# Kernel optimization log

Measured on AMD Instinct MI355X. Metric: run time of the kernel, lower is better.

## Reference

```python
import jax, jax.numpy as jnp
import numpy as np
import math

B, S, D, H = 2, 2048, 1024, 16
DH = D // H  # dim_per_head = 64


def setup_inputs() -> dict:
    key = jax.random.key(0)
    ks = jax.random.split(key, 12)
    s = 1.0 / math.sqrt(D)
    return {
        "key": jax.random.normal(ks[0], (B, S, D), jnp.float32),
        "value": jax.random.normal(ks[1], (B, S, D), jnp.float32),
        "query": jax.random.normal(ks[2], (B, S, D), jnp.float32),
        "mask": jax.random.randint(ks[3], (B, S, S), 0, 2).astype(bool),
        "Wq": jax.random.normal(ks[4], (D, D), jnp.float32) * s,
        "bq": jnp.zeros((D,), jnp.float32),
        "Wk": jax.random.normal(ks[5], (D, D), jnp.float32) * s,
        "bk": jnp.zeros((D,), jnp.float32),
        "Wv": jax.random.normal(ks[6], (D, D), jnp.float32) * s,
        "bv": jnp.zeros((D,), jnp.float32),
        "Wo": jax.random.normal(ks[7], (D, D), jnp.float32) * s,
        "bo": jnp.zeros((D,), jnp.float32),
    }


def _shape(x):
    # [B, S, D] -> [B, H, S, DH]
    return x.reshape(B, -1, H, DH).transpose(0, 2, 1, 3)


def reference(key, value, query, mask, Wq, bq, Wk, bk, Wv, bv, Wo, bo):
    q = _shape(query @ Wq.T + bq)  # [B,H,Sq,DH]
    k = _shape(key @ Wk.T + bk)    # [B,H,Sk,DH]
    v = _shape(value @ Wv.T + bv)  # [B,H,Sk,DH]
    q = q / jnp.sqrt(jnp.asarray(DH, q.dtype))
    scores = jnp.einsum("bhqd,bhkd->bhqk", q, k)
    scores = jnp.where(mask[:, None, :, :], jnp.asarray(-1e18, scores.dtype), scores)
    attn = jax.nn.softmax(scores, axis=-1)
    # dropout is identity in eval/deterministic reference
    ctx = jnp.einsum("bhqk,bhkd->bhqd", attn, v)
    ctx = ctx.transpose(0, 2, 1, 3).reshape(B, -1, D)  # unshape
    return ctx @ Wo.T + bo
```

## Files before the change

### kernel.cpp

```cpp
#include <hip/hip_runtime.h>
#include <math.h>


constexpr int Bc  = 2;
constexpr int Sc  = 2048;
constexpr int Dc  = 1024;
constexpr int Hc  = 16;
constexpr int DHc = 64;
constexpr int BSc = Bc * Sc;

constexpr float LOG2E = 1.4426950408889634f;

typedef __bf16 bf16x8 __attribute__((ext_vector_type(8)));
typedef __bf16 bf16x4 __attribute__((ext_vector_type(4)));
typedef float  f32x4  __attribute__((ext_vector_type(4)));

#define GLDS16(gp, lp) __builtin_amdgcn_global_load_lds( \
    (const __attribute__((address_space(1))) void*)(gp), \
    (__attribute__((address_space(3))) void*)(lp), 16, 0, 0)

__global__ __launch_bounds__(256)
void wsplit(const float* __restrict__ W0, const float* __restrict__ W1,
            const float* __restrict__ W2, const float* __restrict__ W3,
            __bf16* __restrict__ out)
{
    const float* src[4] = {W0, W1, W2, W3};
    const int z = blockIdx.y;
    const size_t idx = ((size_t)blockIdx.x * 256 + threadIdx.x) * 4;
    const float4 v = *(const float4*)&src[z][idx];
    bf16x4 o;
    o[0] = (__bf16)v.x; o[1] = (__bf16)v.y; o[2] = (__bf16)v.z; o[3] = (__bf16)v.w;
    *(bf16x4*)&out[(size_t)z * Dc * Dc + idx] = o;
}

__device__ __forceinline__ void sweep128p(const float* __restrict__ A,
                                          const __bf16* __restrict__ Wh,
                                          char* AsB, char* WsB,
                                          int gm0, int gn0, f32x4 acc[4][4])
{
    const int tid  = threadIdx.x;
    const int w    = tid >> 6;
    const int lane = tid & 63;
    const int cc   = lane & 15;
    const int g    = lane >> 4;
    const int wm   = (w & 1) * 64;
    const int wn   = (w >> 1) * 64;

    int wrow[4], wchk[4];
#pragma unroll
    for (int r = 0; r < 4; ++r) {
        const int L = r * 256 + tid;
        wrow[r] = L >> 3;
        wchk[r] = (L & 7) ^ (wrow[r] & 7);
    }

    float4 av[8];
#pragma unroll
    for (int r = 0; r < 4; ++r)
        GLDS16(Wh + (size_t)(gn0 + wrow[r]) * Dc + wchk[r] * 8,
               WsB + (r * 256 + tid) * 16);
#pragma unroll
    for (int i = 0; i < 8; ++i) {
        const int Lq = i * 256 + tid;
        av[i] = *(const float4*)&A[(size_t)(gm0 + (Lq >> 4)) * Dc + (Lq & 15) * 4];
    }
#pragma unroll
    for (int i = 0; i < 8; ++i) {
        const int Lq = i * 256 + tid;
        const int ar = Lq >> 4, aq = Lq & 15;
        const int off = ar * 128 + ((((aq >> 1) ^ (ar & 7)) << 4) | ((aq & 1) << 3));
        bf16x4 hv;
        hv[0] = (__bf16)av[i].x; hv[1] = (__bf16)av[i].y;
        hv[2] = (__bf16)av[i].z; hv[3] = (__bf16)av[i].w;
        *(bf16x4*)(AsB + off) = hv;
    }

    for (int it = 0; it < Dc / 64; ++it) {
        const char* As = AsB + (it & 1) * 16384;
        const char* Ws = WsB + (it & 1) * 16384;
        __syncthreads();

        const bool more = (it + 1 < Dc / 64);
        if (more) {
            const int kn = (it + 1) * 64;
            char* Wn = WsB + ((it + 1) & 1) * 16384;
#pragma unroll
            for (int r = 0; r < 4; ++r)
                GLDS16(Wh + (size_t)(gn0 + wrow[r]) * Dc + kn + wchk[r] * 8,
                       Wn + (r * 256 + tid) * 16);
#pragma unroll
            for (int i = 0; i < 8; ++i) {
                const int Lq = i * 256 + tid;
                av[i] = *(const float4*)
                    &A[(size_t)(gm0 + (Lq >> 4)) * Dc + kn + (Lq & 15) * 4];
            }
        }

#pragma unroll
        for (int kk = 0; kk < 2; ++kk) {
            const int cb4 = (kk * 4 + g) << 4;
            bf16x8 af[4], bfr[4];
#pragma unroll
            for (int mt = 0; mt < 4; ++mt) {
                const int row = wm + mt * 16 + cc;
                af[mt] = *(const bf16x8*)(As + row * 128 + (cb4 ^ ((row & 7) << 4)));
            }
#pragma unroll
            for (int nt = 0; nt < 4; ++nt) {
                const int row = wn + nt * 16 + cc;
                bfr[nt] = *(const bf16x8*)(Ws + row * 128 + (cb4 ^ ((row & 7) << 4)));
            }
#pragma unroll
            for (int mt = 0; mt < 4; ++mt)
#pragma unroll
                for (int nt = 0; nt < 4; ++nt)
                    acc[mt][nt] = __builtin_amdgcn_mfma_f32_16x16x32_bf16(
                        af[mt], bfr[nt], acc[mt][nt], 0, 0, 0);
        }

        if (more) {
            char* An = AsB + ((it + 1) & 1) * 16384;
#pragma unroll
            for (int i = 0; i < 8; ++i) {
                const int Lq = i * 256 + tid;
                const int ar = Lq >> 4, aq = Lq & 15;
                const int off = ar * 128 +
                                ((((aq >> 1) ^ (ar & 7)) << 4) | ((aq & 1) << 3));
                bf16x4 hv;
                hv[0] = (__bf16)av[i].x; hv[1] = (__bf16)av[i].y;
                hv[2] = (__bf16)av[i].z; hv[3] = (__bf16)av[i].w;
                *(bf16x4*)(An + off) = hv;
            }
        }
    }
}

__device__ __forceinline__ void sweep64p(const __bf16* __restrict__ Ahi,
                                         const __bf16* __restrict__ Alo,
                                         const __bf16* __restrict__ Wh,
                                         char* WsB, char* AhB, char* AlB,
                                         int gm0, int gn0, f32x4 acc[2][4])
{
    const int tid  = threadIdx.x;
    const int w    = tid >> 6;
    const int lane = tid & 63;
    const int cc   = lane & 15;
    const int g    = lane >> 4;
    const int wm   = (w & 1) * 32;
    const int wn   = (w >> 1) * 64;

    int wrow[4], wchk[4];
#pragma unroll
    for (int r = 0; r < 4; ++r) {
        const int L = r * 256 + tid;
        wrow[r] = L >> 3;
        wchk[r] = (L & 7) ^ (wrow[r] & 7);
    }
    int arow[2], achk[2];
#pragma unroll
    for (int r = 0; r < 2; ++r) {
        const int L = r * 256 + tid;
        arow[r] = L >> 3;
        achk[r] = (L & 7) ^ (arow[r] & 7);
    }

#pragma unroll
    for (int r = 0; r < 4; ++r)
        GLDS16(Wh + (size_t)(gn0 + wrow[r]) * Dc + wchk[r] * 8,
               WsB + (r * 256 + tid) * 16);
#pragma unroll
    for (int r = 0; r < 2; ++r) {
        GLDS16(Ahi + (size_t)(gm0 + arow[r]) * Dc + achk[r] * 8,
               AhB + (r * 256 + tid) * 16);
        GLDS16(Alo + (size_t)(gm0 + arow[r]) * Dc + achk[r] * 8,
               AlB + (r * 256 + tid) * 16);
    }

    for (int it = 0; it < Dc / 64; ++it) {
        const char* Ws = WsB + (it & 1) * 16384;
        const char* Ah = AhB + (it & 1) * 8192;
        const char* Al = AlB + (it & 1) * 8192;
        __syncthreads();

        if (it + 1 < Dc / 64) {
            const int kn = (it + 1) * 64;
            char* Wn = WsB + ((it + 1) & 1) * 16384;
            char* Hn = AhB + ((it + 1) & 1) * 8192;
            char* Ln = AlB + ((it + 1) & 1) * 8192;
#pragma unroll
            for (int r = 0; r < 4; ++r)
                GLDS16(Wh + (size_t)(gn0 + wrow[r]) * Dc + kn + wchk[r] * 8,
                       Wn + (r * 256 + tid) * 16);
#pragma unroll
            for (int r = 0; r < 2; ++r) {
                GLDS16(Ahi + (size_t)(gm0 + arow[r]) * Dc + kn + achk[r] * 8,
                       Hn + (r * 256 + tid) * 16);
                GLDS16(Alo + (size_t)(gm0 + arow[r]) * Dc + kn + achk[r] * 8,
                       Ln + (r * 256 + tid) * 16);
            }
        }

#pragma unroll
        for (int kk = 0; kk < 2; ++kk) {
            const int cb4 = (kk * 4 + g) << 4;
            bf16x8 ahi[2], alo[2], bfr[4];
#pragma unroll
            for (int mt = 0; mt < 2; ++mt) {
                const int row = wm + mt * 16 + cc;
                const int off = row * 128 + (cb4 ^ ((row & 7) << 4));
                ahi[mt] = *(const bf16x8*)(Ah + off);
                alo[mt] = *(const bf16x8*)(Al + off);
            }
#pragma unroll
            for (int nt = 0; nt < 4; ++nt) {
                const int row = wn + nt * 16 + cc;
                bfr[nt] = *(const bf16x8*)(Ws + row * 128 + (cb4 ^ ((row & 7) << 4)));
            }
#pragma unroll
            for (int mt = 0; mt < 2; ++mt)
#pragma unroll
                for (int nt = 0; nt < 4; ++nt) {
                    acc[mt][nt] = __builtin_amdgcn_mfma_f32_16x16x32_bf16(
                        ahi[mt], bfr[nt], acc[mt][nt], 0, 0, 0);
                    acc[mt][nt] = __builtin_amdgcn_mfma_f32_16x16x32_bf16(
                        alo[mt], bfr[nt], acc[mt][nt], 0, 0, 0);
                }
        }
    }
}

__global__ __launch_bounds__(256)
void qkv_mfma(const float* __restrict__ query, const float* __restrict__ key,
              const float* __restrict__ value, const __bf16* __restrict__ Whi,
              const float* __restrict__ bq, const float* __restrict__ bk,
              const float* __restrict__ bv,
              __bf16* __restrict__ Qo, __bf16* __restrict__ Ko, __bf16* __restrict__ Vt)
{
    __shared__ __align__(16) char smem[65536];

    const int z = blockIdx.z;
    const float* A    = (z == 0) ? query : (z == 1) ? key : value;
    const float* bias = (z == 0) ? bq    : (z == 1) ? bk  : bv;
    const float scale = (z == 0) ? 0.125f * LOG2E : 1.0f;
    const __bf16* Wh  = Whi + (size_t)z * Dc * Dc;

    const int gm0 = blockIdx.x * 128;
    const int gn0 = blockIdx.y * 128;

    f32x4 acc[4][4];
#pragma unroll
    for (int mt = 0; mt < 4; ++mt)
#pragma unroll
        for (int nt = 0; nt < 4; ++nt) acc[mt][nt] = {0.f, 0.f, 0.f, 0.f};

    sweep128p(A, Wh, smem, smem + 32768, gm0, gn0, acc);

    const int tid = threadIdx.x;
    const int w = tid >> 6, lane = tid & 63;
    const int cc = lane & 15, g = lane >> 4;
    const int wm = (w & 1) * 64, wn = (w >> 1) * 64;

    float bias4[4];
#pragma unroll
    for (int nt = 0; nt < 4; ++nt) bias4[nt] = bias[gn0 + wn + nt * 16 + cc];

    if (z == 2) {
#pragma unroll
        for (int mt = 0; mt < 4; ++mt)
#pragma unroll
            for (int nt = 0; nt < 4; ++nt) {
                const int col = gn0 + wn + nt * 16 + cc;
                const int h = col >> 6, dh = col & 63;
                const int row0 = gm0 + wm + mt * 16 + g * 4;
                const int b = row0 >> 11, s0 = row0 & 2047;
                bf16x4 vv;
#pragma unroll
                for (int reg = 0; reg < 4; ++reg)
                    vv[reg] = (__bf16)(acc[mt][nt][reg] + bias4[nt]);
                *(bf16x4*)&Vt[(((size_t)(b * Hc + h)) * DHc + dh) * Sc + s0] = vv;
            }
    } else {
        __bf16* O = (z == 0) ? Qo : Ko;
#pragma unroll
        for (int mt = 0; mt < 4; ++mt)
#pragma unroll
            for (int nt = 0; nt < 4; ++nt) {
                const int col = gn0 + wn + nt * 16 + cc;
                const int h = col >> 6, dh = col & 63;
#pragma unroll
                for (int reg = 0; reg < 4; ++reg) {
                    const int row = gm0 + wm + mt * 16 + g * 4 + reg;
                    const int b = row >> 11, s = row & 2047;
                    O[(((size_t)(b * Hc + h)) * Sc + s) * DHc + dh] =
                        (__bf16)((acc[mt][nt][reg] + bias4[nt]) * scale);
                }
            }
    }
}

__global__ __launch_bounds__(256)
void out_mfma(const __bf16* __restrict__ ctxHi, const __bf16* __restrict__ ctxLo,
              const __bf16* __restrict__ Wohi,
              const float* __restrict__ bo, float* __restrict__ out)
{
    __shared__ __align__(16) char smem[65536];

    const int gm0 = blockIdx.x * 64;
    const int gn0 = blockIdx.y * 128;

    f32x4 acc[2][4];
#pragma unroll
    for (int mt = 0; mt < 2; ++mt)
#pragma unroll
        for (int nt = 0; nt < 4; ++nt) acc[mt][nt] = {0.f, 0.f, 0.f, 0.f};

    sweep64p(ctxHi, ctxLo, Wohi, smem, smem + 32768, smem + 49152, gm0, gn0, acc);

    const int tid = threadIdx.x;
    const int w = tid >> 6, lane = tid & 63;
    const int cc = lane & 15, g = lane >> 4;
    const int wm = (w & 1) * 32, wn = (w >> 1) * 64;

    float bias4[4];
#pragma unroll
    for (int nt = 0; nt < 4; ++nt) bias4[nt] = bo[gn0 + wn + nt * 16 + cc];

#pragma unroll
    for (int mt = 0; mt < 2; ++mt)
#pragma unroll
        for (int nt = 0; nt < 4; ++nt) {
            const int col = gn0 + wn + nt * 16 + cc;
#pragma unroll
            for (int reg = 0; reg < 4; ++reg) {
                const int row = gm0 + wm + mt * 16 + g * 4 + reg;
                out[(size_t)row * Dc + col] = acc[mt][nt][reg] + bias4[nt];
            }
        }
}

__global__ __launch_bounds__(256)
void mask_pack(const int* __restrict__ mask, unsigned long long* __restrict__ out)
{
    const int lane = threadIdx.x & 63;
    const size_t waveBase = ((size_t)blockIdx.x * 4 + (threadIdx.x >> 6)) * 256;
    unsigned long long b0 = __ballot(mask[waveBase + lane]        != 0);
    unsigned long long b1 = __ballot(mask[waveBase + 64 + lane]   != 0);
    unsigned long long b2 = __ballot(mask[waveBase + 128 + lane]  != 0);
    unsigned long long b3 = __ballot(mask[waveBase + 192 + lane]  != 0);
    if (lane == 0) {
        unsigned long long* dst = out + (waveBase >> 6);
        dst[0] = b0; dst[1] = b1; dst[2] = b2; dst[3] = b3;
    }
}

__global__ __launch_bounds__(256, 2)
void attn_mfma(const __bf16* __restrict__ Q, const __bf16* __restrict__ K,
               const __bf16* __restrict__ Vt,
               const unsigned long long* __restrict__ mp,
               __bf16* __restrict__ ctxHi, __bf16* __restrict__ ctxLo)
{
    __shared__ __align__(16) char smem[40960];

    const int tid  = threadIdx.x;
    const int w    = tid >> 6;
    const int lane = tid & 63;
    const int cc   = lane & 15;
    const int g    = lane >> 4;
    const int bh   = blockIdx.y;
    const int b    = bh >> 4;
    const int h    = bh & 15;
    const int qw   = blockIdx.x * 128 + w * 32;

    const __bf16* Qb  = Q  + (size_t)bh * Sc * DHc;
    const __bf16* Kb  = K  + (size_t)bh * Sc * DHc;
    const __bf16* Vtb = Vt + (size_t)bh * DHc * Sc;

    char* Pw = smem + 32768 + w * 2048;

    bf16x8 qa[2][2];
#pragma unroll
    for (int mt = 0; mt < 2; ++mt) {
        qa[mt][0] = *(const bf16x8*)&Qb[(size_t)(qw + mt * 16 + cc) * DHc + g * 8];
        qa[mt][1] = *(const bf16x8*)&Qb[(size_t)(qw + mt * 16 + cc) * DHc + 32 + g * 8];
    }

    f32x4 o[2][4] = {};
    float l[2][4] = {};

    const int ci[2] = {tid, 256 + tid};
    int  rowi[2], ski[2];
#pragma unroll
    for (int i = 0; i < 2; ++i) {
        rowi[i] = ci[i] >> 3;
        const int sl = ci[i] & 7;
        ski[i] = sl ^ (rowi[i] & 7);
    }

#pragma unroll
    for (int i = 0; i < 2; ++i) {
        GLDS16(Kb + (size_t)rowi[i] * DHc + ski[i] * 8,
               smem + ci[i] * 16);
        GLDS16(Vtb + (size_t)rowi[i] * Sc + ski[i] * 8,
               smem + 8192 + ci[i] * 16);
    }

    for (int it = 0; it < 32; ++it) {
        const int k0 = it * 64;
        char* Ks = smem + (it & 1) * 16384;
        char* Vs = Ks + 8192;

        __syncthreads();

        if (it + 1 < 32) {
            char* Kn = smem + ((it + 1) & 1) * 16384;
            const int kn = k0 + 64;
#pragma unroll
            for (int i = 0; i < 2; ++i) {
                GLDS16(Kb + (size_t)(kn + rowi[i]) * DHc + ski[i] * 8,
                       Kn + ci[i] * 16);
                GLDS16(Vtb + (size_t)rowi[i] * Sc + kn + ski[i] * 8,
                       Kn + 8192 + ci[i] * 16);
            }
        }

        unsigned long long mw[2][4];
#pragma unroll
        for (int mt = 0; mt < 2; ++mt)
#pragma unroll
            for (int r = 0; r < 4; ++r)
                mw[mt][r] = mp[(size_t)(b * Sc + qw + mt * 16 + g * 4 + r) * (Sc / 64)
                               + (k0 >> 6)];

        f32x4 sc[2][4];
#pragma unroll
        for (int nt = 0; nt < 4; ++nt) {
            const int row = nt * 16 + cc;
            const int rx  = (row & 7) << 4;
            const bf16x8 kb0 = *(const bf16x8*)(Ks + row * 128 + ((g << 4) ^ rx));
            const bf16x8 kb1 = *(const bf16x8*)(Ks + row * 128 + ((64 + (g << 4)) ^ rx));
            f32x4 z0 = {-24.f, -24.f, -24.f, -24.f};
            z0 = __builtin_amdgcn_mfma_f32_16x16x32_bf16(qa[0][0], kb0, z0, 0, 0, 0);
            z0 = __builtin_amdgcn_mfma_f32_16x16x32_bf16(qa[0][1], kb1, z0, 0, 0, 0);
            sc[0][nt] = z0;
            f32x4 z1 = {-24.f, -24.f, -24.f, -24.f};
            z1 = __builtin_amdgcn_mfma_f32_16x16x32_bf16(qa[1][0], kb0, z1, 0, 0, 0);
            z1 = __builtin_amdgcn_mfma_f32_16x16x32_bf16(qa[1][1], kb1, z1, 0, 0, 0);
            sc[1][nt] = z1;
        }

        bf16x8 pa[2][2];
#pragma unroll
        for (int mt = 0; mt < 2; ++mt) {
            unsigned mlo[4], mhi[4];
#pragma unroll
            for (int r = 0; r < 4; ++r) {
                const unsigned long long sh = mw[mt][r] >> cc;
                mlo[r] = (unsigned)sh;
                mhi[r] = (unsigned)(sh >> 32);
            }
#pragma unroll
            for (int nt = 0; nt < 4; ++nt)
#pragma unroll
                for (int r = 0; r < 4; ++r) {
                    float p = __builtin_amdgcn_exp2f(sc[mt][nt][r]);
                    const unsigned bit =
                        (nt == 0) ? (mlo[r] & 1u) :
                        (nt == 1) ? (mlo[r] & 0x10000u) :
                        (nt == 2) ? (mhi[r] & 1u) : (mhi[r] & 0x10000u);
                    p = bit ? 0.f : p;
                    l[mt][r] += p;
                    *(__bf16*)(Pw + (g * 4 + r) * 128 +
                               (((nt ^ g) << 5) | (cc << 1))) = (__bf16)p;
                }
            const int sw = (cc >> 2) << 5;
            pa[mt][0] = *(const bf16x8*)(Pw + cc * 128 + ((g * 16) ^ sw));
            pa[mt][1] = *(const bf16x8*)(Pw + cc * 128 + ((64 + g * 16) ^ sw));
        }

#pragma unroll
        for (int nt = 0; nt < 4; ++nt) {
            const int row = nt * 16 + cc;
            const int rx  = (row & 7) << 4;
            const bf16x8 vb0 = *(const bf16x8*)(Vs + row * 128 + ((g << 4) ^ rx));
            const bf16x8 vb1 = *(const bf16x8*)(Vs + row * 128 + ((64 + (g << 4)) ^ rx));
            o[0][nt] = __builtin_amdgcn_mfma_f32_16x16x32_bf16(pa[0][0], vb0, o[0][nt], 0, 0, 0);
            o[0][nt] = __builtin_amdgcn_mfma_f32_16x16x32_bf16(pa[0][1], vb1, o[0][nt], 0, 0, 0);
            o[1][nt] = __builtin_amdgcn_mfma_f32_16x16x32_bf16(pa[1][0], vb0, o[1][nt], 0, 0, 0);
            o[1][nt] = __builtin_amdgcn_mfma_f32_16x16x32_bf16(pa[1][1], vb1, o[1][nt], 0, 0, 0);
        }
    }

#pragma unroll
    for (int off = 1; off < 16; off <<= 1)
#pragma unroll
        for (int mt = 0; mt < 2; ++mt)
#pragma unroll
            for (int r = 0; r < 4; ++r)
                l[mt][r] += __shfl_xor(l[mt][r], off, 16);

#pragma unroll
    for (int mt = 0; mt < 2; ++mt)
#pragma unroll
        for (int r = 0; r < 4; ++r) {
            const float inv = 1.0f / l[mt][r];
            const int q = qw + mt * 16 + g * 4 + r;
#pragma unroll
            for (int nt = 0; nt < 4; ++nt) {
                const size_t idx = ((size_t)b * Sc + q) * Dc + h * 64 + nt * 16 + cc;
                const float v = o[mt][nt][r] * inv;
                const __bf16 hi = (__bf16)v;
                ctxHi[idx] = hi;
                ctxLo[idx] = (__bf16)(v - (float)hi);
            }
        }
}

extern "C" void kernel_launch(void* const* d_in, const int* in_sizes, int n_in,
                              void* d_out, int out_size, void* d_ws, size_t ws_size,
                              hipStream_t stream)
{
    const float* key   = (const float*)d_in[0];
    const float* value = (const float*)d_in[1];
    const float* query = (const float*)d_in[2];
    const int*   mask  = (const int*)  d_in[3];
    const float* Wq    = (const float*)d_in[4];
    const float* bq    = (const float*)d_in[5];
    const float* Wk    = (const float*)d_in[6];
    const float* bk    = (const float*)d_in[7];
    const float* Wv    = (const float*)d_in[8];
    const float* bv    = (const float*)d_in[9];
    const float* Wo    = (const float*)d_in[10];
    const float* bo    = (const float*)d_in[11];
    float* out = (float*)d_out;

    char* wsb = (char*)d_ws;
    __bf16* Qbf  = (__bf16*)(wsb);
    __bf16* Kbf  = (__bf16*)(wsb + ((size_t)8  << 20));
    __bf16* Vt   = (__bf16*)(wsb + ((size_t)16 << 20));
    unsigned long long* mpk = (unsigned long long*)(wsb + ((size_t)32 << 20));
    __bf16* Whi  = (__bf16*)(wsb + ((size_t)33 << 20));
    __bf16* ctxHi = (__bf16*)(wsb + ((size_t)41 << 20));
    __bf16* ctxLo = (__bf16*)(wsb + ((size_t)49 << 20));

    dim3 gws(Dc * Dc / (256 * 4), 4);
    wsplit<<<gws, 256, 0, stream>>>(Wq, Wk, Wv, Wo, Whi);

    dim3 gqkv(BSc / 128, Dc / 128, 3);
    qkv_mfma<<<gqkv, 256, 0, stream>>>(query, key, value, Whi, bq, bk, bv,
                                       Qbf, Kbf, Vt);

    const int mask_n = Bc * Sc * Sc;
    mask_pack<<<mask_n / 1024, 256, 0, stream>>>(mask, mpk);

    dim3 gattn(Sc / 128, Bc * Hc);
    attn_mfma<<<gattn, 256, 0, stream>>>(Qbf, Kbf, Vt, mpk, ctxHi, ctxLo);

    dim3 gout(BSc / 64, Dc / 128);
    out_mfma<<<gout, 256, 0, stream>>>(ctxHi, ctxLo, Whi + (size_t)3 * Dc * Dc,
                                       bo, out);
}
```

Baseline: 282.2 us.

## Halve attention query tile per block and permute K rows for packed P stores

The attention kernel now gives each wave 16 query rows instead of 32, so each block covers 64 queries. The grid doubles and the launch bound allows 4 blocks per CU, aiming at higher occupancy and better latency hiding. K rows are loaded into LDS in a permuted order so that each lane's four score columns map to four consecutive keys. That lets the mask take one 4-bit nibble per lane and lets P be written as packed bf16x4 stores with a new XOR swizzle. The cost is that K/V tiles are fetched from global/L2 twice as often per query, and each wave does less MFMA work per LDS read.

```diff
diff --git a/kernel.cpp b/kernel.cpp
--- a/kernel.cpp
+++ b/kernel.cpp
@@ -353,7 +353,7 @@
     }
 }
 
-__global__ __launch_bounds__(256, 2)
+__global__ __launch_bounds__(256, 4)
 void attn_mfma(const __bf16* __restrict__ Q, const __bf16* __restrict__ K,
                const __bf16* __restrict__ Vt,
                const unsigned long long* __restrict__ mp,
@@ -369,7 +369,7 @@
     const int bh   = blockIdx.y;
     const int b    = bh >> 4;
     const int h    = bh & 15;
-    const int qw   = blockIdx.x * 128 + w * 32;
+    const int qw   = blockIdx.x * 64 + w * 16;
 
     const __bf16* Qb  = Q  + (size_t)bh * Sc * DHc;
     const __bf16* Kb  = K  + (size_t)bh * Sc * DHc;
@@ -377,28 +377,29 @@
 
     char* Pw = smem + 32768 + w * 2048;
 
-    bf16x8 qa[2][2];
-#pragma unroll
-    for (int mt = 0; mt < 2; ++mt) {
-        qa[mt][0] = *(const bf16x8*)&Qb[(size_t)(qw + mt * 16 + cc) * DHc + g * 8];
-        qa[mt][1] = *(const bf16x8*)&Qb[(size_t)(qw + mt * 16 + cc) * DHc + 32 + g * 8];
-    }
-
-    f32x4 o[2][4] = {};
-    float l[2][4] = {};
+    bf16x8 qa[2];
+    qa[0] = *(const bf16x8*)&Qb[(size_t)(qw + cc) * DHc + g * 8];
+    qa[1] = *(const bf16x8*)&Qb[(size_t)(qw + cc) * DHc + 32 + g * 8];
+
+    f32x4 o[4] = {};
+    float l[4] = {};
 
     const int ci[2] = {tid, 256 + tid};
-    int  rowi[2], ski[2];
+    int  rowi[2], ski[2], krow[2];
 #pragma unroll
     for (int i = 0; i < 2; ++i) {
         rowi[i] = ci[i] >> 3;
         const int sl = ci[i] & 7;
-        ski[i] = sl ^ (rowi[i] & 7);
-    }
+        ski[i]  = sl ^ (rowi[i] & 7);
+        krow[i] = ((rowi[i] & 15) << 2) | (rowi[i] >> 4);
+    }
+
+    const int pswW = ((( (g * 4) ^ ((g * 4) >> 3)) & 7) << 4);
+    const int pswR = (((cc ^ (cc >> 3)) & 7) << 4);
 
 #pragma unroll
     for (int i = 0; i < 2; ++i) {
-        GLDS16(Kb + (size_t)rowi[i] * DHc + ski[i] * 8,
+        GLDS16(Kb + (size_t)krow[i] * DHc + ski[i] * 8,
                smem + ci[i] * 16);
         GLDS16(Vtb + (size_t)rowi[i] * Sc + ski[i] * 8,
                smem + 8192 + ci[i] * 16);
@@ -416,66 +417,49 @@
             const int kn = k0 + 64;
 #pragma unroll
             for (int i = 0; i < 2; ++i) {
-                GLDS16(Kb + (size_t)(kn + rowi[i]) * DHc + ski[i] * 8,
+                GLDS16(Kb + (size_t)(kn + krow[i]) * DHc + ski[i] * 8,
                        Kn + ci[i] * 16);
                 GLDS16(Vtb + (size_t)rowi[i] * Sc + kn + ski[i] * 8,
                        Kn + 8192 + ci[i] * 16);
             }
         }
 
-        unsigned long long mw[2][4];
-#pragma unroll
-        for (int mt = 0; mt < 2; ++mt)
-#pragma unroll
-            for (int r = 0; r < 4; ++r)
-                mw[mt][r] = mp[(size_t)(b * Sc + qw + mt * 16 + g * 4 + r) * (Sc / 64)
-                               + (k0 >> 6)];
-
-        f32x4 sc[2][4];
+        unsigned long long mw[4];
+#pragma unroll
+        for (int r = 0; r < 4; ++r)
+            mw[r] = mp[(size_t)(b * Sc + qw + g * 4 + r) * (Sc / 64) + (k0 >> 6)];
+
+        f32x4 sc[4];
 #pragma unroll
         for (int nt = 0; nt < 4; ++nt) {
             const int row = nt * 16 + cc;
             const int rx  = (row & 7) << 4;
             const bf16x8 kb0 = *(const bf16x8*)(Ks + row * 128 + ((g << 4) ^ rx));
             const bf16x8 kb1 = *(const bf16x8*)(Ks + row * 128 + ((64 + (g << 4)) ^ rx));
-            f32x4 z0 = {-24.f, -24.f, -24.f, -24.f};
-            z0 = __builtin_amdgcn_mfma_f32_16x16x32_bf16(qa[0][0], kb0, z0, 0, 0, 0);
-            z0 = __builtin_amdgcn_mfma_f32_16x16x32_bf16(qa[0][1], kb1, z0, 0, 0, 0);
-            sc[0][nt] = z0;
-            f32x4 z1 = {-24.f, -24.f, -24.f, -24.f};
-            z1 = __builtin_amdgcn_mfma_f32_16x16x32_bf16(qa[1][0], kb0, z1, 0, 0, 0);
-            z1 = __builtin_amdgcn_mfma_f32_16x16x32_bf16(qa[1][1], kb1, z1, 0, 0, 0);
-            sc[1][nt] = z1;
-        }
-
-        bf16x8 pa[2][2];
-#pragma unroll
-        for (int mt = 0; mt < 2; ++mt) {
-            unsigned mlo[4], mhi[4];
-#pragma unroll
-            for (int r = 0; r < 4; ++r) {
-                const unsigned long long sh = mw[mt][r] >> cc;
-                mlo[r] = (unsigned)sh;
-                mhi[r] = (unsigned)(sh >> 32);
-            }
-#pragma unroll
-            for (int nt = 0; nt < 4; ++nt)
-#pragma unroll
-                for (int r = 0; r < 4; ++r) {
-                    float p = __builtin_amdgcn_exp2f(sc[mt][nt][r]);
-                    const unsigned bit =
-                        (nt == 0) ? (mlo[r] & 1u) :
-                        (nt == 1) ? (mlo[r] & 0x10000u) :
-                        (nt == 2) ? (mhi[r] & 1u) : (mhi[r] & 0x10000u);
-                    p = bit ? 0.f : p;
-                    l[mt][r] += p;
-                    *(__bf16*)(Pw + (g * 4 + r) * 128 +
-                               (((nt ^ g) << 5) | (cc << 1))) = (__bf16)p;
-                }
-            const int sw = (cc >> 2) << 5;
-            pa[mt][0] = *(const bf16x8*)(Pw + cc * 128 + ((g * 16) ^ sw));
-            pa[mt][1] = *(const bf16x8*)(Pw + cc * 128 + ((64 + g * 16) ^ sw));
-        }
+            f32x4 z = {-24.f, -24.f, -24.f, -24.f};
+            z = __builtin_amdgcn_mfma_f32_16x16x32_bf16(qa[0], kb0, z, 0, 0, 0);
+            z = __builtin_amdgcn_mfma_f32_16x16x32_bf16(qa[1], kb1, z, 0, 0, 0);
+            sc[nt] = z;
+        }
+
+        bf16x8 pa[2];
+#pragma unroll
+        for (int r = 0; r < 4; ++r) {
+            const unsigned s4 = (unsigned)(mw[r] >> (cc * 4)) & 0xFu;
+            bf16x4 pv;
+#pragma unroll
+            for (int nt = 0; nt < 4; ++nt) {
+                float p = __builtin_amdgcn_exp2f(sc[nt][r]);
+                p = (s4 & (1u << nt)) ? 0.f : p;
+                l[r] += p;
+                pv[nt] = (__bf16)p;
+            }
+            const int prow = g * 4 + r;
+            const int psw  = (((prow ^ (prow >> 3)) & 7) << 4);
+            *(bf16x4*)(Pw + prow * 128 + ((8 * cc) ^ psw)) = pv;
+        }
+        pa[0] = *(const bf16x8*)(Pw + cc * 128 + ((16 * g) ^ pswR));
+        pa[1] = *(const bf16x8*)(Pw + cc * 128 + ((64 + 16 * g) ^ pswR));
 
 #pragma unroll
         for (int nt = 0; nt < 4; ++nt) {
@@ -483,36 +467,32 @@
             const int rx  = (row & 7) << 4;
             const bf16x8 vb0 = *(const bf16x8*)(Vs + row * 128 + ((g << 4) ^ rx));
             const bf16x8 vb1 = *(const bf16x8*)(Vs + row * 128 + ((64 + (g << 4)) ^ rx));
-            o[0][nt] = __builtin_amdgcn_mfma_f32_16x16x32_bf16(pa[0][0], vb0, o[0][nt], 0, 0, 0);
-            o[0][nt] = __builtin_amdgcn_mfma_f32_16x16x32_bf16(pa[0][1], vb1, o[0][nt], 0, 0, 0);
-            o[1][nt] = __builtin_amdgcn_mfma_f32_16x16x32_bf16(pa[1][0], vb0, o[1][nt], 0, 0, 0);
-            o[1][nt] = __builtin_amdgcn_mfma_f32_16x16x32_bf16(pa[1][1], vb1, o[1][nt], 0, 0, 0);
-        }
-    }
+            o[nt] = __builtin_amdgcn_mfma_f32_16x16x32_bf16(pa[0], vb0, o[nt], 0, 0, 0);
+            o[nt] = __builtin_amdgcn_mfma_f32_16x16x32_bf16(pa[1], vb1, o[nt], 0, 0, 0);
+        }
+    }
+
+    (void)pswW;
 
 #pragma unroll
     for (int off = 1; off < 16; off <<= 1)
 #pragma unroll
-        for (int mt = 0; mt < 2; ++mt)
-#pragma unroll
-            for (int r = 0; r < 4; ++r)
-                l[mt][r] += __shfl_xor(l[mt][r], off, 16);
-
-#pragma unroll
-    for (int mt = 0; mt < 2; ++mt)
-#pragma unroll
-        for (int r = 0; r < 4; ++r) {
-            const float inv = 1.0f / l[mt][r];
-            const int q = qw + mt * 16 + g * 4 + r;
-#pragma unroll
-            for (int nt = 0; nt < 4; ++nt) {
-                const size_t idx = ((size_t)b * Sc + q) * Dc + h * 64 + nt * 16 + cc;
-                const float v = o[mt][nt][r] * inv;
-                const __bf16 hi = (__bf16)v;
-                ctxHi[idx] = hi;
-                ctxLo[idx] = (__bf16)(v - (float)hi);
-            }
-        }
+        for (int r = 0; r < 4; ++r)
+            l[r] += __shfl_xor(l[r], off, 16);
+
+#pragma unroll
+    for (int r = 0; r < 4; ++r) {
+        const float inv = 1.0f / l[r];
+        const int q = qw + g * 4 + r;
+#pragma unroll
+        for (int nt = 0; nt < 4; ++nt) {
+            const size_t idx = ((size_t)b * Sc + q) * Dc + h * 64 + nt * 16 + cc;
+            const float v = o[nt][r] * inv;
+            const __bf16 hi = (__bf16)v;
+            ctxHi[idx] = hi;
+            ctxLo[idx] = (__bf16)(v - (float)hi);
+        }
+    }
 }
 
 extern "C" void kernel_launch(void* const* d_in, const int* in_sizes, int n_in,
@@ -552,7 +532,7 @@
     const int mask_n = Bc * Sc * Sc;
     mask_pack<<<mask_n / 1024, 256, 0, stream>>>(mask, mpk);
 
-    dim3 gattn(Sc / 128, Bc * Hc);
+    dim3 gattn(Sc / 64, Bc * Hc);
     attn_mfma<<<gattn, 256, 0, stream>>>(Qbf, Kbf, Vt, mpk, ctxHi, ctxLo);
 
     dim3 gout(BSc / 64, Dc / 128);
```

New measurement: 280.0 us. Within noise of the previous version (-0.8%).
